# Kernel optimization log

Measured on AMD Instinct MI355X. Metric: run time of the kernel, lower is better.

The kernel has to match this reference:

```python
import jax, jax.numpy as jnp
import numpy as np

B, T, N = 128, 256, 128   # batch, input suffix (query positions), bunch size
ATTN_DIM, VEC_DIM = 512, 512
NEG_INF = -1e30


def setup_inputs() -> dict:
    key = jax.random.key(0)
    k1, k2, k3, k4, k5, k6, k7 = jax.random.split(key, 7)
    inputs = jax.random.normal(k1, (B, T, VEC_DIM), dtype=jnp.float32)
    attend_over = jax.random.normal(k2, (B, N, ATTN_DIM), dtype=jnp.float32)
    attend_mask = jax.random.randint(k3, (B, N), 0, 2) > 0
    # kaiming-uniform-ish init for bi_weight (fan_in = vec_dim)
    bound = float(np.sqrt(1.0 / VEC_DIM))
    bi_weight = jax.random.uniform(k4, (ATTN_DIM, VEC_DIM), minval=-bound, maxval=bound, dtype=jnp.float32)
    a_w = jax.random.uniform(k5, (ATTN_DIM,), minval=-bound, maxval=bound, dtype=jnp.float32)
    b_w = jax.random.uniform(k6, (VEC_DIM,), minval=-bound, maxval=bound, dtype=jnp.float32)
    bias = jax.random.uniform(k7, (1,), minval=-bound, maxval=bound, dtype=jnp.float32)
    return {"inputs": inputs, "attend_over": attend_over, "attend_mask": attend_mask,
            "bi_weight": bi_weight, "a_w": a_w, "b_w": b_w, "bias": bias}


def reference(inputs, attend_over, attend_mask, bi_weight, a_w, b_w, bias):
    # bilinear score: a^T M b  -> (B, T, N)
    aM = jnp.einsum('bna,av->bnv', attend_over, bi_weight)          # (B, N, VEC)
    sim = jnp.einsum('btv,bnv->btn', inputs, aM)                    # (B, T, N)
    # linear terms: w_a^T a  and  w_b^T b
    lin_a = jnp.einsum('bna,a->bn', attend_over, a_w)               # (B, N)
    lin_b = jnp.einsum('btv,v->bt', inputs, b_w)                    # (B, T)
    sim = sim + lin_a[:, None, :] + lin_b[:, :, None] + bias[0]
    sim = jnp.tanh(sim)
    # masked softmax over the bunch dim N
    masked = jnp.where(attend_mask[:, None, :], sim, NEG_INF)
    attn = jax.nn.softmax(masked, axis=-1)                          # (B, T, N)
    attn = attn * attend_mask[:, None, :].astype(attn.dtype)
    # weighted sum of attended vectors -> context (B, T, ATTN_DIM)
    context = jnp.einsum('btn,bna->bta', attn, attend_over)
    return context
```

## Files before the change

kernel.cpp:

```cpp
#include <hip/hip_runtime.h>

#define Bsz 128
#define Tsz 256
#define Nsz 128
#define Asz 512
#define Vsz 512
#define LIN_BLOCKS 12288

typedef __attribute__((ext_vector_type(8))) short bh8;
typedef __attribute__((ext_vector_type(4))) float f32x4;

__device__ __forceinline__ unsigned short f2bf(float x) {
  unsigned int u = __float_as_uint(x);
  return (unsigned short)((u + 0x7fffu + ((u >> 16) & 1u)) >> 16);
}
__device__ __forceinline__ float bf2f(unsigned short h) {
  return __uint_as_float(((unsigned int)h) << 16);
}
__device__ __forceinline__ float fast_tanh(float x) {
  float ax = fabsf(x);
  float e = __expf(-2.f * ax);
  float t = (1.f - e) / (1.f + e);
  return copysignf(t, x);
}

__device__ __forceinline__ void gld16(const void* g, void* l) {
  __builtin_amdgcn_global_load_lds(
      (const __attribute__((address_space(1))) unsigned int*)g,
      (__attribute__((address_space(3))) unsigned int*)l, 16, 0, 0);
}

struct Frag2 { bh8 hi, lo; };
__device__ __forceinline__ Frag2 load_split8(const float* p) {
  float4 x0 = *(const float4*)p;
  float4 x1 = *(const float4*)(p + 4);
  float xs[8] = {x0.x, x0.y, x0.z, x0.w, x1.x, x1.y, x1.z, x1.w};
  union { unsigned int u[4]; bh8 v; } H, L;
#pragma unroll
  for (int i = 0; i < 4; ++i) {
    unsigned int a = __float_as_uint(xs[2 * i]);
    unsigned int b = __float_as_uint(xs[2 * i + 1]);
    H.u[i] = (a >> 16) | (b & 0xffff0000u);
    float la = xs[2 * i]     - __uint_as_float(a & 0xffff0000u);
    float lb = xs[2 * i + 1] - __uint_as_float(b & 0xffff0000u);
    L.u[i] = (__float_as_uint(la) >> 16) | (__float_as_uint(lb) & 0xffff0000u);
  }
  Frag2 r; r.hi = H.v; r.lo = L.v; return r;
}

__global__ __launch_bounds__(256) void prep(
    const float* __restrict__ AO, const float* __restrict__ inputs,
    const float* __restrict__ W, const float* __restrict__ a_w,
    const float* __restrict__ b_w, float* __restrict__ lin_a,
    float* __restrict__ lin_b, unsigned short* __restrict__ WT_hi,
    unsigned short* __restrict__ WT_lo)
{
  __shared__ float t[64][65];
  int tid = threadIdx.x;
  if (blockIdx.x < LIN_BLOCKS) {
    int gw = (blockIdx.x * 256 + tid) >> 6;
    int lane = tid & 63;
    const float* src; const float* w; float* dst;
    if (gw < Bsz * Nsz) { src = AO + (long)gw * Asz; w = a_w; dst = lin_a + gw; }
    else { int r = gw - Bsz * Nsz; src = inputs + (long)r * Vsz; w = b_w; dst = lin_b + r; }
    float4 x0 = *(const float4*)(src + lane * 4);
    float4 x1 = *(const float4*)(src + 256 + lane * 4);
    float4 w0 = *(const float4*)(w + lane * 4);
    float4 w1 = *(const float4*)(w + 256 + lane * 4);
    float d = x0.x*w0.x + x0.y*w0.y + x0.z*w0.z + x0.w*w0.w
            + x1.x*w1.x + x1.y*w1.y + x1.z*w1.z + x1.w*w1.w;
#pragma unroll
    for (int off = 32; off; off >>= 1) d += __shfl_xor(d, off);
    if (lane == 0) *dst = d;
  } else {
    int bb = blockIdx.x - LIN_BLOCKS;
    int a0 = (bb & 7) * 64, v0 = (bb >> 3) * 64;
#pragma unroll
    for (int l = 0; l < 4; ++l) {
      int idx = tid + l * 256;
      int r = idx >> 4, c = (idx & 15) * 4;
      float4 v = *(const float4*)(W + (long)(a0 + r) * Vsz + v0 + c);
      t[r][c] = v.x; t[r][c+1] = v.y; t[r][c+2] = v.z; t[r][c+3] = v.w;
    }
    __syncthreads();
#pragma unroll
    for (int l = 0; l < 4; ++l) {
      int idx = tid + l * 256;
      int r = idx >> 4, c = (idx & 15) * 4;
      ushort4 h, lo;
      unsigned short* hp = (unsigned short*)&h;
      unsigned short* lp = (unsigned short*)&lo;
#pragma unroll
      for (int j = 0; j < 4; ++j) {
        float x = t[c + j][r];
        hp[j] = f2bf(x);
        lp[j] = f2bf(x - bf2f(hp[j]));
      }
      *(ushort4*)&WT_hi[(long)(v0 + r) * Asz + a0 + c] = h;
      *(ushort4*)&WT_lo[(long)(v0 + r) * Asz + a0 + c] = lo;
    }
  }
}

__global__ __launch_bounds__(256) void gemm_aM(
    const float* __restrict__ AO, const unsigned short* __restrict__ WT_hi,
    const unsigned short* __restrict__ WT_lo,
    unsigned short* __restrict__ aM_hi, unsigned short* __restrict__ aM_lo)
{
  __shared__ unsigned short b_hi[128][32];
  __shared__ unsigned short b_lo[128][32];
  int tid = threadIdx.x;
  int wave = tid >> 6, lane = tid & 63;
  int wr = wave >> 1, wc = wave & 1;
  int lr = lane & 15, kg = lane >> 4;
  long m0 = (long)blockIdx.x * 128;
  int  n0 = blockIdx.y * 128;
  f32x4 acc[4][4] = {};
  for (int k0 = 0; k0 < Asz; k0 += 32) {
#pragma unroll
    for (int rep = 0; rep < 2; ++rep) {
      int seg = wave + rep * 4;
      int i = seg * 64 + lane;
      int r = i >> 2, c8 = (i & 3) * 8;
      long off = (long)(n0 + r) * Asz + k0 + c8;
      gld16(WT_hi + off, (char*)&b_hi[0][0] + seg * 1024);
      gld16(WT_lo + off, (char*)&b_lo[0][0] + seg * 1024);
    }
    Frag2 a[4];
#pragma unroll
    for (int m = 0; m < 4; ++m)
      a[m] = load_split8(AO + (m0 + wr * 64 + m * 16 + lr) * Asz + k0 + kg * 8);
    __syncthreads();
    bh8 bh_[4], bl[4];
#pragma unroll
    for (int n = 0; n < 4; ++n) {
      bh_[n] = *(const bh8*)&b_hi[wc * 64 + n * 16 + lr][kg * 8];
      bl[n]  = *(const bh8*)&b_lo[wc * 64 + n * 16 + lr][kg * 8];
    }
#pragma unroll
    for (int m = 0; m < 4; ++m)
#pragma unroll
      for (int n = 0; n < 4; ++n) {
        acc[m][n] = __builtin_amdgcn_mfma_f32_16x16x32_bf16(a[m].hi, bh_[n], acc[m][n], 0, 0, 0);
        acc[m][n] = __builtin_amdgcn_mfma_f32_16x16x32_bf16(a[m].hi, bl[n],  acc[m][n], 0, 0, 0);
        acc[m][n] = __builtin_amdgcn_mfma_f32_16x16x32_bf16(a[m].lo, bh_[n], acc[m][n], 0, 0, 0);
      }
    __syncthreads();
  }
#pragma unroll
  for (int m = 0; m < 4; ++m)
#pragma unroll
    for (int n = 0; n < 4; ++n)
#pragma unroll
      for (int j = 0; j < 4; ++j) {
        float x = acc[m][n][j];
        unsigned int u = __float_as_uint(x);
        unsigned short h = (unsigned short)(u >> 16);
        float lof = x - __uint_as_float(u & 0xffff0000u);
        unsigned short l = (unsigned short)(__float_as_uint(lof) >> 16);
        long row = m0 + wr * 64 + m * 16 + kg * 4 + j;
        int  col = n0 + wc * 64 + n * 16 + lr;
        aM_hi[row * Asz + col] = h;
        aM_lo[row * Asz + col] = l;
      }
}

__global__ __launch_bounds__(512) void sim_fused(
    const float* __restrict__ inputs, const unsigned short* __restrict__ aMh,
    const unsigned short* __restrict__ aMl, const float* __restrict__ lin_a,
    const float* __restrict__ lin_b, const int* __restrict__ mask,
    const float* __restrict__ bias, unsigned short* __restrict__ attn_bf)
{
  __shared__ union SU {
    struct { unsigned short b_hi[128][32], b_lo[128][32]; } st;
    float S[64][132];
  } u;
  int b = blockIdx.y;
  int t0 = blockIdx.x * 64;
  int tid = threadIdx.x;
  int wave = tid >> 6, lane = tid & 63;
  int wr = wave >> 2, wc = wave & 3;
  int lr = lane & 15, kg = lane >> 4;
  const float* Ap = inputs + ((long)b * Tsz + t0) * Vsz;
  const unsigned short* Bh = aMh + (long)b * Nsz * Vsz;
  const unsigned short* Bl = aMl + (long)b * Nsz * Vsz;
  f32x4 acc[2][2] = {};
  for (int k0 = 0; k0 < Vsz; k0 += 32) {
    {
      int i = wave * 64 + lane;
      int r = i >> 2, c8 = (i & 3) * 8;
      long off = (long)r * Vsz + k0 + c8;
      gld16(Bh + off, (char*)&u.st.b_hi[0][0] + wave * 1024);
      gld16(Bl + off, (char*)&u.st.b_lo[0][0] + wave * 1024);
    }
    Frag2 a[2];
#pragma unroll
    for (int m = 0; m < 2; ++m)
      a[m] = load_split8(Ap + (long)(wr * 32 + m * 16 + lr) * Vsz + k0 + kg * 8);
    __syncthreads();
    bh8 bh_[2], bl[2];
#pragma unroll
    for (int n = 0; n < 2; ++n) {
      bh_[n] = *(const bh8*)&u.st.b_hi[wc * 32 + n * 16 + lr][kg * 8];
      bl[n]  = *(const bh8*)&u.st.b_lo[wc * 32 + n * 16 + lr][kg * 8];
    }
#pragma unroll
    for (int m = 0; m < 2; ++m)
#pragma unroll
      for (int n = 0; n < 2; ++n) {
        acc[m][n] = __builtin_amdgcn_mfma_f32_16x16x32_bf16(a[m].hi, bh_[n], acc[m][n], 0, 0, 0);
        acc[m][n] = __builtin_amdgcn_mfma_f32_16x16x32_bf16(a[m].hi, bl[n],  acc[m][n], 0, 0, 0);
        acc[m][n] = __builtin_amdgcn_mfma_f32_16x16x32_bf16(a[m].lo, bh_[n], acc[m][n], 0, 0, 0);
      }
    __syncthreads();
  }
#pragma unroll
  for (int m = 0; m < 2; ++m)
#pragma unroll
    for (int n = 0; n < 2; ++n)
#pragma unroll
      for (int j = 0; j < 4; ++j)
        u.S[wr * 32 + m * 16 + kg * 4 + j][wc * 32 + n * 16 + lr] = acc[m][n][j];
  __syncthreads();

  float la0 = lin_a[b * Nsz + lane];
  float la1 = lin_a[b * Nsz + 64 + lane];
  int   mk0 = mask[b * Nsz + lane];
  int   mk1 = mask[b * Nsz + 64 + lane];
  float bs  = bias[0];
#pragma unroll
  for (int rr = 0; rr < 8; ++rr) {
    int r = wave * 8 + rr;
    int tI = t0 + r;
    float lb = lin_b[b * Tsz + tI] + bs;
    float s0 = u.S[r][lane] + la0 + lb;
    float s1 = u.S[r][64 + lane] + la1 + lb;
    s0 = fast_tanh(s0); s1 = fast_tanh(s1);
    float v0 = mk0 ? s0 : -1e30f;
    float v1 = mk1 ? s1 : -1e30f;
    float mx = fmaxf(v0, v1);
#pragma unroll
    for (int off = 32; off; off >>= 1) mx = fmaxf(mx, __shfl_xor(mx, off));
    float e0 = mk0 ? __expf(v0 - mx) : 0.f;
    float e1 = mk1 ? __expf(v1 - mx) : 0.f;
    float sm = e0 + e1;
#pragma unroll
    for (int off = 32; off; off >>= 1) sm += __shfl_xor(sm, off);
    float inv = 1.f / sm;
    long base = ((long)b * Tsz + tI) * Nsz;
    attn_bf[base + lane]      = f2bf(e0 * inv);
    attn_bf[base + 64 + lane] = f2bf(e1 * inv);
  }
}

__global__ __launch_bounds__(256) void ao_transpose(
    const float* __restrict__ AO, unsigned short* __restrict__ AOt)
{
  __shared__ unsigned short t[128][128];
  int b = blockIdx.x >> 2;
  int a0 = (blockIdx.x & 3) * 128;
  int tid = threadIdx.x;
#pragma unroll
  for (int l = 0; l < 16; ++l) {
    int idx = tid + l * 256;
    int r = idx >> 5, c = (idx & 31) * 4;
    float4 v = *(const float4*)(AO + ((long)b * Nsz + r) * Asz + a0 + c);
    ushort4 h;
    unsigned short* hp = (unsigned short*)&h;
    hp[0] = f2bf(v.x); hp[1] = f2bf(v.y); hp[2] = f2bf(v.z); hp[3] = f2bf(v.w);
    int key = ((r >> 3) & 7) << 2;
    *(ushort4*)&t[r][c ^ key] = h;
  }
  __syncthreads();
#pragma unroll
  for (int l = 0; l < 8; ++l) {
    int idx = tid + l * 256;
    int ra = idx >> 4, cc = idx & 15;
    int key = (cc & 7) << 2;
    union { unsigned short s[8]; uint4 q; } g;
#pragma unroll
    for (int j = 0; j < 8; ++j) g.s[j] = t[cc * 8 + j][ra ^ key];
    *(uint4*)&AOt[((long)b * Asz + a0 + ra) * Nsz + cc * 8] = g.q;
  }
}

__global__ __launch_bounds__(256) void gemm_ctx(
    const unsigned short* __restrict__ attn_bf, const unsigned short* __restrict__ AOt,
    float* __restrict__ out)
{
  __shared__ unsigned short a_t[128][32];
  __shared__ unsigned short b_t[128][32];
  int b = blockIdx.z;
  int m0 = blockIdx.x * 128, n0 = blockIdx.y * 128;
  int tid = threadIdx.x;
  int wave = tid >> 6, lane = tid & 63;
  int wr = wave >> 1, wc = wave & 1;
  int lr = lane & 15, kg = lane >> 4;
  const unsigned short* Ap = attn_bf + (long)b * Tsz * Nsz;
  const unsigned short* Bp = AOt + (long)b * Asz * Nsz;
  f32x4 acc[4][4] = {};
  for (int k0 = 0; k0 < Nsz; k0 += 32) {
#pragma unroll
    for (int rep = 0; rep < 2; ++rep) {
      int seg = wave + rep * 4;
      int i = seg * 64 + lane;
      int r = i >> 2, c8 = (i & 3) * 8;
      gld16(Ap + (long)(m0 + r) * Nsz + k0 + c8, (char*)&a_t[0][0] + seg * 1024);
      gld16(Bp + (long)(n0 + r) * Nsz + k0 + c8, (char*)&b_t[0][0] + seg * 1024);
    }
    __syncthreads();
    bh8 af[4], bf_[4];
#pragma unroll
    for (int m = 0; m < 4; ++m) af[m] = *(const bh8*)&a_t[wr * 64 + m * 16 + lr][kg * 8];
#pragma unroll
    for (int n = 0; n < 4; ++n) bf_[n] = *(const bh8*)&b_t[wc * 64 + n * 16 + lr][kg * 8];
#pragma unroll
    for (int m = 0; m < 4; ++m)
#pragma unroll
      for (int n = 0; n < 4; ++n)
        acc[m][n] = __builtin_amdgcn_mfma_f32_16x16x32_bf16(af[m], bf_[n], acc[m][n], 0, 0, 0);
    __syncthreads();
  }
#pragma unroll
  for (int m = 0; m < 4; ++m)
#pragma unroll
    for (int n = 0; n < 4; ++n)
#pragma unroll
      for (int j = 0; j < 4; ++j)
        out[((long)b * Tsz + m0 + wr * 64 + m * 16 + kg * 4 + j) * Asz + n0 + wc * 64 + n * 16 + lr]
          = acc[m][n][j];
}

extern "C" void kernel_launch(void* const* d_in, const int* in_sizes, int n_in,
                              void* d_out, int out_size, void* d_ws, size_t ws_size,
                              hipStream_t stream) {
  const float* inputs = (const float*)d_in[0];
  const float* AO     = (const float*)d_in[1];
  const int*   mask   = (const int*)d_in[2];
  const float* W      = (const float*)d_in[3];
  const float* a_w    = (const float*)d_in[4];
  const float* b_w    = (const float*)d_in[5];
  const float* bias   = (const float*)d_in[6];
  float* out = (float*)d_out;
  char* wsb  = (char*)d_ws;

  unsigned short* aM_hi   = (unsigned short*)wsb;
  unsigned short* aM_lo   = (unsigned short*)(wsb + 16777216);
  unsigned short* AOt     = (unsigned short*)wsb;
  unsigned short* WT_hi   = (unsigned short*)(wsb + 33554432);
  unsigned short* WT_lo   = (unsigned short*)(wsb + 34078720);
  float*          lin_a   = (float*)(wsb + 34603008);
  float*          lin_b   = (float*)(wsb + 34668544);
  unsigned short* attn_bf = (unsigned short*)(wsb + 34799616);

  prep<<<LIN_BLOCKS + 64, 256, 0, stream>>>(AO, inputs, W, a_w, b_w, lin_a, lin_b, WT_hi, WT_lo);
  gemm_aM<<<dim3(128, 4), 256, 0, stream>>>(AO, WT_hi, WT_lo, aM_hi, aM_lo);
  sim_fused<<<dim3(4, 128), 512, 0, stream>>>(inputs, aM_hi, aM_lo, lin_a, lin_b, mask, bias, attn_bf);
  ao_transpose<<<512, 256, 0, stream>>>(AO, AOt);
  gemm_ctx<<<dim3(2, 4, 128), 256, 0, stream>>>(attn_bf, AOt, out);
}
```

Baseline: 265.6 us.

## Fuse linear-term dot products into GEMMs, swizzle LDS, and retile aM/sim kernels

Removes the separate pass that computed lin_a and lin_b. lin_a is now accumulated inside gemm_aM from the AO fragments it already loads, and lin_b inside sim_fused from the input fragments, so activations are no longer re-read from global memory just for those dot products. All three MFMA kernels get an XOR swizzle on their LDS tile columns to reduce bank conflicts. gemm_aM's M tile is halved to 64 and sim_fused's T tile to 32 with 256 threads, doubling both grids, which adds redundant reads of the aM tiles per batch.

Result: slower. 273.0 us (+2.8%).

```diff
diff --git a/kernel.cpp b/kernel.cpp
--- a/kernel.cpp
+++ b/kernel.cpp
@@ -5,7 +5,6 @@
 #define Nsz 128
 #define Asz 512
 #define Vsz 512
-#define LIN_BLOCKS 12288
 
 typedef __attribute__((ext_vector_type(8))) short bh8;
 typedef __attribute__((ext_vector_type(4))) float f32x4;
@@ -31,9 +30,7 @@
 }
 
 struct Frag2 { bh8 hi, lo; };
-__device__ __forceinline__ Frag2 load_split8(const float* p) {
-  float4 x0 = *(const float4*)p;
-  float4 x1 = *(const float4*)(p + 4);
+__device__ __forceinline__ Frag2 split8(float4 x0, float4 x1) {
   float xs[8] = {x0.x, x0.y, x0.z, x0.w, x1.x, x1.y, x1.z, x1.w};
   union { unsigned int u[4]; bh8 v; } H, L;
 #pragma unroll
@@ -47,65 +44,50 @@
   }
   Frag2 r; r.hi = H.v; r.lo = L.v; return r;
 }
-
-__global__ __launch_bounds__(256) void prep(
-    const float* __restrict__ AO, const float* __restrict__ inputs,
-    const float* __restrict__ W, const float* __restrict__ a_w,
-    const float* __restrict__ b_w, float* __restrict__ lin_a,
-    float* __restrict__ lin_b, unsigned short* __restrict__ WT_hi,
+__device__ __forceinline__ float dot8(float4 x0, float4 x1, float4 w0, float4 w1) {
+  return x0.x*w0.x + x0.y*w0.y + x0.z*w0.z + x0.w*w0.w
+       + x1.x*w1.x + x1.y*w1.y + x1.z*w1.z + x1.w*w1.w;
+}
+
+__global__ __launch_bounds__(256) void prep_wt(
+    const float* __restrict__ W, unsigned short* __restrict__ WT_hi,
     unsigned short* __restrict__ WT_lo)
 {
   __shared__ float t[64][65];
   int tid = threadIdx.x;
-  if (blockIdx.x < LIN_BLOCKS) {
-    int gw = (blockIdx.x * 256 + tid) >> 6;
-    int lane = tid & 63;
-    const float* src; const float* w; float* dst;
-    if (gw < Bsz * Nsz) { src = AO + (long)gw * Asz; w = a_w; dst = lin_a + gw; }
-    else { int r = gw - Bsz * Nsz; src = inputs + (long)r * Vsz; w = b_w; dst = lin_b + r; }
-    float4 x0 = *(const float4*)(src + lane * 4);
-    float4 x1 = *(const float4*)(src + 256 + lane * 4);
-    float4 w0 = *(const float4*)(w + lane * 4);
-    float4 w1 = *(const float4*)(w + 256 + lane * 4);
-    float d = x0.x*w0.x + x0.y*w0.y + x0.z*w0.z + x0.w*w0.w
-            + x1.x*w1.x + x1.y*w1.y + x1.z*w1.z + x1.w*w1.w;
-#pragma unroll
-    for (int off = 32; off; off >>= 1) d += __shfl_xor(d, off);
-    if (lane == 0) *dst = d;
-  } else {
-    int bb = blockIdx.x - LIN_BLOCKS;
-    int a0 = (bb & 7) * 64, v0 = (bb >> 3) * 64;
-#pragma unroll
-    for (int l = 0; l < 4; ++l) {
-      int idx = tid + l * 256;
-      int r = idx >> 4, c = (idx & 15) * 4;
-      float4 v = *(const float4*)(W + (long)(a0 + r) * Vsz + v0 + c);
-      t[r][c] = v.x; t[r][c+1] = v.y; t[r][c+2] = v.z; t[r][c+3] = v.w;
-    }
-    __syncthreads();
-#pragma unroll
-    for (int l = 0; l < 4; ++l) {
-      int idx = tid + l * 256;
-      int r = idx >> 4, c = (idx & 15) * 4;
-      ushort4 h, lo;
-      unsigned short* hp = (unsigned short*)&h;
-      unsigned short* lp = (unsigned short*)&lo;
-#pragma unroll
-      for (int j = 0; j < 4; ++j) {
-        float x = t[c + j][r];
-        hp[j] = f2bf(x);
-        lp[j] = f2bf(x - bf2f(hp[j]));
-      }
-      *(ushort4*)&WT_hi[(long)(v0 + r) * Asz + a0 + c] = h;
-      *(ushort4*)&WT_lo[(long)(v0 + r) * Asz + a0 + c] = lo;
-    }
+  int bb = blockIdx.x;
+  int a0 = (bb & 7) * 64, v0 = (bb >> 3) * 64;
+#pragma unroll
+  for (int l = 0; l < 4; ++l) {
+    int idx = tid + l * 256;
+    int r = idx >> 4, c = (idx & 15) * 4;
+    float4 v = *(const float4*)(W + (long)(a0 + r) * Vsz + v0 + c);
+    t[r][c] = v.x; t[r][c+1] = v.y; t[r][c+2] = v.z; t[r][c+3] = v.w;
+  }
+  __syncthreads();
+#pragma unroll
+  for (int l = 0; l < 4; ++l) {
+    int idx = tid + l * 256;
+    int r = idx >> 4, c = (idx & 15) * 4;
+    ushort4 h, lo;
+    unsigned short* hp = (unsigned short*)&h;
+    unsigned short* lp = (unsigned short*)&lo;
+#pragma unroll
+    for (int j = 0; j < 4; ++j) {
+      float x = t[c + j][r];
+      hp[j] = f2bf(x);
+      lp[j] = f2bf(x - bf2f(hp[j]));
+    }
+    *(ushort4*)&WT_hi[(long)(v0 + r) * Asz + a0 + c] = h;
+    *(ushort4*)&WT_lo[(long)(v0 + r) * Asz + a0 + c] = lo;
   }
 }
 
 __global__ __launch_bounds__(256) void gemm_aM(
     const float* __restrict__ AO, const unsigned short* __restrict__ WT_hi,
-    const unsigned short* __restrict__ WT_lo,
-    unsigned short* __restrict__ aM_hi, unsigned short* __restrict__ aM_lo)
+    const unsigned short* __restrict__ WT_lo, const float* __restrict__ a_w,
+    unsigned short* __restrict__ aM_hi, unsigned short* __restrict__ aM_lo,
+    float* __restrict__ lin_a)
 {
   __shared__ unsigned short b_hi[128][32];
   __shared__ unsigned short b_lo[128][32];
@@ -113,32 +95,45 @@
   int wave = tid >> 6, lane = tid & 63;
   int wr = wave >> 1, wc = wave & 1;
   int lr = lane & 15, kg = lane >> 4;
-  long m0 = (long)blockIdx.x * 128;
+  long m0 = (long)blockIdx.x * 64;
   int  n0 = blockIdx.y * 128;
-  f32x4 acc[4][4] = {};
+  bool doLin = (blockIdx.y == 0);
+  f32x4 acc[2][4] = {};
+  float lin[2] = {0.f, 0.f};
   for (int k0 = 0; k0 < Asz; k0 += 32) {
 #pragma unroll
     for (int rep = 0; rep < 2; ++rep) {
-      int seg = wave + rep * 4;
-      int i = seg * 64 + lane;
-      int r = i >> 2, c8 = (i & 3) * 8;
-      long off = (long)(n0 + r) * Asz + k0 + c8;
-      gld16(WT_hi + off, (char*)&b_hi[0][0] + seg * 1024);
-      gld16(WT_lo + off, (char*)&b_lo[0][0] + seg * 1024);
-    }
-    Frag2 a[4];
-#pragma unroll
-    for (int m = 0; m < 4; ++m)
-      a[m] = load_split8(AO + (m0 + wr * 64 + m * 16 + lr) * Asz + k0 + kg * 8);
+      int i = rep * 256 + tid;
+      int r = i >> 2, c8 = i & 3;
+      int cs = (c8 ^ ((r >> 1) & 3)) * 8;
+      long off = (long)(n0 + r) * Asz + k0 + cs;
+      gld16(WT_hi + off, (char*)&b_hi[0][0] + (rep * 4 + wave) * 1024);
+      gld16(WT_lo + off, (char*)&b_lo[0][0] + (rep * 4 + wave) * 1024);
+    }
+    float4 aw0 = {0,0,0,0}, aw1 = {0,0,0,0};
+    if (doLin) {
+      aw0 = *(const float4*)(a_w + k0 + kg * 8);
+      aw1 = *(const float4*)(a_w + k0 + kg * 8 + 4);
+    }
+    Frag2 a[2];
+#pragma unroll
+    for (int m = 0; m < 2; ++m) {
+      const float* p = AO + (m0 + wr * 32 + m * 16 + lr) * Asz + k0 + kg * 8;
+      float4 x0 = *(const float4*)p, x1 = *(const float4*)(p + 4);
+      a[m] = split8(x0, x1);
+      if (doLin) lin[m] += dot8(x0, x1, aw0, aw1);
+    }
     __syncthreads();
     bh8 bh_[4], bl[4];
 #pragma unroll
     for (int n = 0; n < 4; ++n) {
-      bh_[n] = *(const bh8*)&b_hi[wc * 64 + n * 16 + lr][kg * 8];
-      bl[n]  = *(const bh8*)&b_lo[wc * 64 + n * 16 + lr][kg * 8];
-    }
-#pragma unroll
-    for (int m = 0; m < 4; ++m)
+      int row = wc * 64 + n * 16 + lr;
+      int cs = (kg ^ ((lr >> 1) & 3)) * 8;
+      bh_[n] = *(const bh8*)&b_hi[row][cs];
+      bl[n]  = *(const bh8*)&b_lo[row][cs];
+    }
+#pragma unroll
+    for (int m = 0; m < 2; ++m)
 #pragma unroll
       for (int n = 0; n < 4; ++n) {
         acc[m][n] = __builtin_amdgcn_mfma_f32_16x16x32_bf16(a[m].hi, bh_[n], acc[m][n], 0, 0, 0);
@@ -147,8 +142,17 @@
       }
     __syncthreads();
   }
-#pragma unroll
-  for (int m = 0; m < 4; ++m)
+  if (doLin) {
+#pragma unroll
+    for (int m = 0; m < 2; ++m) {
+      float v = lin[m];
+      v += __shfl_xor(v, 16);
+      v += __shfl_xor(v, 32);
+      if (wc == 0 && lane < 16) lin_a[m0 + wr * 32 + m * 16 + lr] = v;
+    }
+  }
+#pragma unroll
+  for (int m = 0; m < 2; ++m)
 #pragma unroll
     for (int n = 0; n < 4; ++n)
 #pragma unroll
@@ -158,69 +162,81 @@
         unsigned short h = (unsigned short)(u >> 16);
         float lof = x - __uint_as_float(u & 0xffff0000u);
         unsigned short l = (unsigned short)(__float_as_uint(lof) >> 16);
-        long row = m0 + wr * 64 + m * 16 + kg * 4 + j;
+        long row = m0 + wr * 32 + m * 16 + kg * 4 + j;
         int  col = n0 + wc * 64 + n * 16 + lr;
         aM_hi[row * Asz + col] = h;
         aM_lo[row * Asz + col] = l;
       }
 }
 
-__global__ __launch_bounds__(512) void sim_fused(
+__global__ __launch_bounds__(256) void sim_fused(
     const float* __restrict__ inputs, const unsigned short* __restrict__ aMh,
     const unsigned short* __restrict__ aMl, const float* __restrict__ lin_a,
-    const float* __restrict__ lin_b, const int* __restrict__ mask,
+    const float* __restrict__ b_w, const int* __restrict__ mask,
     const float* __restrict__ bias, unsigned short* __restrict__ attn_bf)
 {
   __shared__ union SU {
     struct { unsigned short b_hi[128][32], b_lo[128][32]; } st;
-    float S[64][132];
+    float S[32][132];
   } u;
+  __shared__ float linb_s[32];
   int b = blockIdx.y;
-  int t0 = blockIdx.x * 64;
+  int t0 = blockIdx.x * 32;
   int tid = threadIdx.x;
   int wave = tid >> 6, lane = tid & 63;
-  int wr = wave >> 2, wc = wave & 3;
+  int wr = wave >> 1, wc = wave & 1;
   int lr = lane & 15, kg = lane >> 4;
   const float* Ap = inputs + ((long)b * Tsz + t0) * Vsz;
   const unsigned short* Bh = aMh + (long)b * Nsz * Vsz;
   const unsigned short* Bl = aMl + (long)b * Nsz * Vsz;
-  f32x4 acc[2][2] = {};
+  f32x4 acc[4] = {};
+  float linb = 0.f;
   for (int k0 = 0; k0 < Vsz; k0 += 32) {
-    {
-      int i = wave * 64 + lane;
-      int r = i >> 2, c8 = (i & 3) * 8;
-      long off = (long)r * Vsz + k0 + c8;
-      gld16(Bh + off, (char*)&u.st.b_hi[0][0] + wave * 1024);
-      gld16(Bl + off, (char*)&u.st.b_lo[0][0] + wave * 1024);
-    }
-    Frag2 a[2];
-#pragma unroll
-    for (int m = 0; m < 2; ++m)
-      a[m] = load_split8(Ap + (long)(wr * 32 + m * 16 + lr) * Vsz + k0 + kg * 8);
-    __syncthreads();
-    bh8 bh_[2], bl[2];
-#pragma unroll
-    for (int n = 0; n < 2; ++n) {
-      bh_[n] = *(const bh8*)&u.st.b_hi[wc * 32 + n * 16 + lr][kg * 8];
-      bl[n]  = *(const bh8*)&u.st.b_lo[wc * 32 + n * 16 + lr][kg * 8];
-    }
-#pragma unroll
-    for (int m = 0; m < 2; ++m)
-#pragma unroll
-      for (int n = 0; n < 2; ++n) {
-        acc[m][n] = __builtin_amdgcn_mfma_f32_16x16x32_bf16(a[m].hi, bh_[n], acc[m][n], 0, 0, 0);
-        acc[m][n] = __builtin_amdgcn_mfma_f32_16x16x32_bf16(a[m].hi, bl[n],  acc[m][n], 0, 0, 0);
-        acc[m][n] = __builtin_amdgcn_mfma_f32_16x16x32_bf16(a[m].lo, bh_[n], acc[m][n], 0, 0, 0);
-      }
-    __syncthreads();
-  }
-#pragma unroll
-  for (int m = 0; m < 2; ++m)
-#pragma unroll
-    for (int n = 0; n < 2; ++n)
-#pragma unroll
-      for (int j = 0; j < 4; ++j)
-        u.S[wr * 32 + m * 16 + kg * 4 + j][wc * 32 + n * 16 + lr] = acc[m][n][j];
+#pragma unroll
+    for (int rep = 0; rep < 2; ++rep) {
+      int i = rep * 256 + tid;
+      int r = i >> 2, c8 = i & 3;
+      int cs = (c8 ^ ((r >> 1) & 3)) * 8;
+      long off = (long)r * Vsz + k0 + cs;
+      gld16(Bh + off, (char*)&u.st.b_hi[0][0] + (rep * 4 + wave) * 1024);
+      gld16(Bl + off, (char*)&u.st.b_lo[0][0] + (rep * 4 + wave) * 1024);
+    }
+    const float* p = Ap + (long)(wr * 16 + lr) * Vsz + k0 + kg * 8;
+    float4 x0 = *(const float4*)p, x1 = *(const float4*)(p + 4);
+    Frag2 a = split8(x0, x1);
+    if (wc == 0) {
+      float4 bw0 = *(const float4*)(b_w + k0 + kg * 8);
+      float4 bw1 = *(const float4*)(b_w + k0 + kg * 8 + 4);
+      linb += dot8(x0, x1, bw0, bw1);
+    }
+    __syncthreads();
+    bh8 bh_[4], bl[4];
+#pragma unroll
+    for (int n = 0; n < 4; ++n) {
+      int row = wc * 64 + n * 16 + lr;
+      int cs = (kg ^ ((lr >> 1) & 3)) * 8;
+      bh_[n] = *(const bh8*)&u.st.b_hi[row][cs];
+      bl[n]  = *(const bh8*)&u.st.b_lo[row][cs];
+    }
+#pragma unroll
+    for (int n = 0; n < 4; ++n) {
+      acc[n] = __builtin_amdgcn_mfma_f32_16x16x32_bf16(a.hi, bh_[n], acc[n], 0, 0, 0);
+      acc[n] = __builtin_amdgcn_mfma_f32_16x16x32_bf16(a.hi, bl[n],  acc[n], 0, 0, 0);
+      acc[n] = __builtin_amdgcn_mfma_f32_16x16x32_bf16(a.lo, bh_[n], acc[n], 0, 0, 0);
+    }
+    __syncthreads();
+  }
+  if (wc == 0) {
+    float v = linb;
+    v += __shfl_xor(v, 16);
+    v += __shfl_xor(v, 32);
+    if (lane < 16) linb_s[wr * 16 + lr] = v;
+  }
+#pragma unroll
+  for (int n = 0; n < 4; ++n)
+#pragma unroll
+    for (int j = 0; j < 4; ++j)
+      u.S[wr * 16 + kg * 4 + j][wc * 64 + n * 16 + lr] = acc[n][j];
   __syncthreads();
 
   float la0 = lin_a[b * Nsz + lane];
@@ -232,7 +248,7 @@
   for (int rr = 0; rr < 8; ++rr) {
     int r = wave * 8 + rr;
     int tI = t0 + r;
-    float lb = lin_b[b * Tsz + tI] + bs;
+    float lb = linb_s[r] + bs;
     float s0 = u.S[r][lane] + la0 + lb;
     float s1 = u.S[r][64 + lane] + la1 + lb;
     s0 = fast_tanh(s0); s1 = fast_tanh(s1);
@@ -302,18 +318,19 @@
   for (int k0 = 0; k0 < Nsz; k0 += 32) {
 #pragma unroll
     for (int rep = 0; rep < 2; ++rep) {
-      int seg = wave + rep * 4;
-      int i = seg * 64 + lane;
-      int r = i >> 2, c8 = (i & 3) * 8;
-      gld16(Ap + (long)(m0 + r) * Nsz + k0 + c8, (char*)&a_t[0][0] + seg * 1024);
-      gld16(Bp + (long)(n0 + r) * Nsz + k0 + c8, (char*)&b_t[0][0] + seg * 1024);
+      int i = rep * 256 + tid;
+      int r = i >> 2, c8 = i & 3;
+      int cs = (c8 ^ ((r >> 1) & 3)) * 8;
+      gld16(Ap + (long)(m0 + r) * Nsz + k0 + cs, (char*)&a_t[0][0] + (rep * 4 + wave) * 1024);
+      gld16(Bp + (long)(n0 + r) * Nsz + k0 + cs, (char*)&b_t[0][0] + (rep * 4 + wave) * 1024);
     }
     __syncthreads();
     bh8 af[4], bf_[4];
-#pragma unroll
-    for (int m = 0; m < 4; ++m) af[m] = *(const bh8*)&a_t[wr * 64 + m * 16 + lr][kg * 8];
-#pragma unroll
-    for (int n = 0; n < 4; ++n) bf_[n] = *(const bh8*)&b_t[wc * 64 + n * 16 + lr][kg * 8];
+    int cs = (kg ^ ((lr >> 1) & 3)) * 8;
+#pragma unroll
+    for (int m = 0; m < 4; ++m) af[m] = *(const bh8*)&a_t[wr * 64 + m * 16 + lr][cs];
+#pragma unroll
+    for (int n = 0; n < 4; ++n) bf_[n] = *(const bh8*)&b_t[wc * 64 + n * 16 + lr][cs];
 #pragma unroll
     for (int m = 0; m < 4; ++m)
 #pragma unroll
@@ -350,12 +367,11 @@
   unsigned short* WT_hi   = (unsigned short*)(wsb + 33554432);
   unsigned short* WT_lo   = (unsigned short*)(wsb + 34078720);
   float*          lin_a   = (float*)(wsb + 34603008);
-  float*          lin_b   = (float*)(wsb + 34668544);
   unsigned short* attn_bf = (unsigned short*)(wsb + 34799616);
 
-  prep<<<LIN_BLOCKS + 64, 256, 0, stream>>>(AO, inputs, W, a_w, b_w, lin_a, lin_b, WT_hi, WT_lo);
-  gemm_aM<<<dim3(128, 4), 256, 0, stream>>>(AO, WT_hi, WT_lo, aM_hi, aM_lo);
-  sim_fused<<<dim3(4, 128), 512, 0, stream>>>(inputs, aM_hi, aM_lo, lin_a, lin_b, mask, bias, attn_bf);
+  prep_wt<<<64, 256, 0, stream>>>(W, WT_hi, WT_lo);
+  gemm_aM<<<dim3(256, 4), 256, 0, stream>>>(AO, WT_hi, WT_lo, a_w, aM_hi, aM_lo, lin_a);
+  sim_fused<<<dim3(8, 128), 256, 0, stream>>>(inputs, aM_hi, aM_lo, lin_a, b_w, mask, bias, attn_bf);
   ao_transpose<<<512, 256, 0, stream>>>(AO, AOt);
   gemm_ctx<<<dim3(2, 4, 128), 256, 0, stream>>>(attn_bf, AOt, out);
 }
```
